# Performance work log

Hardware: AMD Instinct MI355X
Metric: run time of the kernel (lower is better)

The kernel has to match this reference:

```python
import jax, jax.numpy as jnp
import numpy as np


def setup_inputs() -> dict:
    key = jax.random.key(0)
    k1, k2, k3, k4, k5 = jax.random.split(key, 5)
    N, C, H, W = 1, 256, 336, 336
    R, P = 256, 7
    features = jax.random.normal(k1, (N, C, H, W), dtype=jnp.float32)
    # ROIs: integer [x1, y1, x2, y2]; width/height in [P, 63] so every bin is non-empty,
    # and boxes stay inside the feature map.
    x1 = jax.random.randint(k2, (R,), 0, H - 64)
    y1 = jax.random.randint(k3, (R,), 0, H - 64)
    w = jax.random.randint(k4, (R,), P, 64)
    h = jax.random.randint(k5, (R,), P, 64)
    rois = jnp.stack([x1, y1, x1 + w, y1 + h], axis=1).astype(jnp.int32)
    return {"features": features, "rois": rois, "output_size": P}


def _bin_index(lo, size, P, L):
    """For each roi, map every coordinate in [0, L) to its bin index in [0, P), or P if outside.

    Boundaries replicate: int(x1 + (width / P) * w) with float32 division and
    truncation (coords are non-negative, so trunc == floor).
    lo, size: [R] float32.  Returns [R, L] int32.
    """
    ws = jnp.arange(P + 1, dtype=jnp.float32)
    b = jnp.floor(lo[:, None] + (size / P)[:, None] * ws[None, :]).astype(jnp.int32)  # [R, P+1]
    j = jnp.arange(L, dtype=jnp.int32)
    # bin index = number of interior boundaries b[1..P] that are <= j
    cnt = jnp.sum((j[None, None, :] >= b[:, 1:, None]).astype(jnp.int32), axis=1)  # [R, L]
    return jnp.where(j[None, :] < b[:, :1], P, cnt)


def reference(features, rois, output_size):
    P = output_size
    feat = features[0]  # [C, H, W]  (original code requires N == 1)
    C, H, W = feat.shape
    x1 = rois[:, 0].astype(jnp.float32)
    y1 = rois[:, 1].astype(jnp.float32)
    rw = jnp.maximum(rois[:, 2] - rois[:, 0] + 1, 1).astype(jnp.float32)
    rh = jnp.maximum(rois[:, 3] - rois[:, 1] + 1, 1).astype(jnp.float32)
    col_bin = _bin_index(x1, rw, P, W)  # [R, W]
    row_bin = _bin_index(y1, rh, P, H)  # [R, H]

    def pool_one(cb, rb):
        # reduce columns into width-bins: [W, C, H] -> [P+1, C, H], drop 'outside' segment
        t = jax.ops.segment_max(jnp.moveaxis(feat, 2, 0), cb, num_segments=P + 1)[:P]  # [Pw, C, H]
        # reduce rows into height-bins: [H, Pw, C] -> [P+1, Pw, C]
        t = jax.ops.segment_max(jnp.moveaxis(t, 2, 0), rb, num_segments=P + 1)[:P]  # [Ph, Pw, C]
        return jnp.transpose(t, (2, 0, 1))  # [C, Ph, Pw]

    return jax.vmap(pool_one)(col_bin, row_bin)  # [R, C, P, P]
```

## Files before the change

kernel.cpp:

```cpp
#include <hip/hip_runtime.h>
#include <math.h>


#define POOL_P 7

__device__ __forceinline__ float4 max4(float4 a, float4 b) {
  return make_float4(fmaxf(a.x, b.x), fmaxf(a.y, b.y),
                     fmaxf(a.z, b.z), fmaxf(a.w, b.w));
}

__global__ __launch_bounds__(64, 4) void roipool_kernel(
    const float* __restrict__ feat, const int* __restrict__ rois,
    float* __restrict__ out, int C, int H, int W, int R) {
  const int x  = blockIdx.x & 7;
  const int s  = blockIdx.x >> 3;
  const int pass = s / (2 * R);
  const int t    = s - pass * 2 * R;
  const int r    = t >> 1;
  const int half = t & 1;
  const int cg8  = (pass << 3) | x;

  const int lane = threadIdx.x;
  const int k  = lane >> 4;
  const int li = lane & 15;
  const int c0 = (cg8 << 3) + (half << 2);

  const int4 roi = *reinterpret_cast<const int4*>(rois + 4 * r);
  const int x1 = roi.x, y1 = roi.y;
  const int rw = max(roi.z - x1 + 1, 1);
  const int rh = max(roi.w - y1 + 1, 1);
  const int x2 = x1 + rw - 1;

  const float sx = __fdiv_rn((float)rw, (float)POOL_P);
  const float sy = __fdiv_rn((float)rh, (float)POOL_P);
  const float x1f = (float)x1, y1f = (float)y1;

  const int xa = x1 & ~3;
  const bool tailc = (x2 >= xa + 64);
  const int lslot = min((x2 - xa) >> 2, 15);

  const size_t HW = (size_t)H * W;
  const int W4 = W >> 2;
  const float* fck = feat + (size_t)(c0 + k) * HW;
  const float4* pmb = reinterpret_cast<const float4*>(fck + xa) + li;
  const float* pt  = fck + xa + 64;

  __shared__ float stg[4][POOL_P][80];

  const float NEG = -__builtin_inff();

  if (li <= lslot) {
    int hprev = y1;
#pragma unroll
    for (int ph = 0; ph < POOL_P; ++ph) {
      const int hend = (int)__fadd_rn(y1f, __fmul_rn(sy, (float)(ph + 1)));
      const int cnt = hend - hprev;
      const int e84 = (cnt - 1) * 84;
      const float4* q = pmb + (size_t)hprev * W4;
      hprev = hend;
      float4 m = q[0];
      m = max4(m, q[min(84,  e84)]);
      m = max4(m, q[min(168, e84)]);
      m = max4(m, q[min(252, e84)]);
      if (cnt > 4) {
        float4 a = q[336];
        float4 b = q[min(420, e84)];
        float4 c = q[min(504, e84)];
        float4 d = q[min(588, e84)];
        m = max4(m, max4(max4(a, b), max4(c, d)));
      }
      if (cnt > 8) {
        const float4* qq = q + 672;
        for (int h = 8; h < cnt; ++h) { m = max4(m, qq[0]); qq += 84; }
      }
      *reinterpret_cast<float4*>(&stg[k][ph][li << 2]) = m;
    }
  }

  if (tailc && li == 0) {
    int hprev = y1;
#pragma unroll
    for (int ph = 0; ph < POOL_P; ++ph) {
      const int hend = (int)__fadd_rn(y1f, __fmul_rn(sy, (float)(ph + 1)));
      float4 tm = make_float4(NEG, NEG, NEG, NEG);
      for (int h = hprev; h < hend; ++h)
        tm = max4(tm, *reinterpret_cast<const float4*>(pt + (size_t)h * W));
      hprev = hend;
      *reinterpret_cast<float4*>(&stg[k][ph][64]) = tm;
    }
  }

  const size_t ob = ((size_t)r * C + c0) * (POOL_P * POOL_P);
#pragma unroll
  for (int i = lane; i < 4 * POOL_P * POOL_P; i += 64) {
    const int k2 = i / (POOL_P * POOL_P);
    const int j  = i - k2 * (POOL_P * POOL_P);
    const int ph = j / POOL_P;
    const int pw = j - ph * POOL_P;
    const int w0 = (int)__fadd_rn(x1f, __fmul_rn(sx, (float)pw)) - xa;
    const int w1 = (int)__fadd_rn(x1f, __fmul_rn(sx, (float)(pw + 1))) - xa;
    const int a0 = w0 & ~3;
    const float* sq = &stg[k2][ph][a0];
    float4 t0 = *reinterpret_cast<const float4*>(sq);
    float4 t1 = *reinterpret_cast<const float4*>(sq + 4);
    float4 t2 = *reinterpret_cast<const float4*>(sq + 8);
    float4 t3 = *reinterpret_cast<const float4*>(sq + 12);
    const int lo = w0 - a0, hi = w1 - a0;
    float e[16] = {t0.x, t0.y, t0.z, t0.w, t1.x, t1.y, t1.z, t1.w,
                   t2.x, t2.y, t2.z, t2.w, t3.x, t3.y, t3.z, t3.w};
    float m = NEG;
#pragma unroll
    for (int jj = 0; jj < 16; ++jj) {
      const float v = (jj >= lo && jj < hi) ? e[jj] : NEG;
      m = fmaxf(m, v);
    }
    out[ob + i] = m;
  }
}

extern "C" void kernel_launch(void* const* d_in, const int* in_sizes, int n_in,
                              void* d_out, int out_size, void* d_ws, size_t ws_size,
                              hipStream_t stream) {
  const float* feat = (const float*)d_in[0];
  const int*   rois = (const int*)d_in[1];
  float*       out  = (float*)d_out;

  const int C = 256, H = 336, W = 336;
  const int R = in_sizes[1] / 4;

  const int n_cg8 = C / 8;
  dim3 grid(n_cg8 * R * 2), block(64);
  roipool_kernel<<<grid, block, 0, stream>>>(feat, rois, out, C, H, W, R);
}
```

Baseline: 51.06 us.

## Stream ROI rows through an LDS ring with async global_load_lds prefetch

Replaces per-bin direct float4 global loads with a 16-slot LDS ring filled by global_load_lds, keeping 13 rows in flight and counting them with explicit vmcnt waits. Rows are max-reduced as they arrive, and each height bin's width reduction runs as soon as that bin finishes, so the old final pass over a staging array goes away. The aim is to hide memory latency with deeper, steadier prefetch. It removes the lslot guard, so all 16 column slots load even when the ROI is narrow, adding extra traffic. It also relies on hand-placed waitcnts with no barriers, which is fragile within a single wave.

```diff
diff --git a/kernel.cpp b/kernel.cpp
--- a/kernel.cpp
+++ b/kernel.cpp
@@ -3,6 +3,9 @@
 
 
 #define POOL_P 7
+
+typedef __attribute__((address_space(1))) const void gld_src_t;
+typedef __attribute__((address_space(3))) void gld_dst_t;
 
 __device__ __forceinline__ float4 max4(float4 a, float4 b) {
   return make_float4(fmaxf(a.x, b.x), fmaxf(a.y, b.y),
@@ -37,84 +40,98 @@
 
   const int xa = x1 & ~3;
   const bool tailc = (x2 >= xa + 64);
-  const int lslot = min((x2 - xa) >> 2, 15);
 
   const size_t HW = (size_t)H * W;
-  const int W4 = W >> 2;
   const float* fck = feat + (size_t)(c0 + k) * HW;
-  const float4* pmb = reinterpret_cast<const float4*>(fck + xa) + li;
-  const float* pt  = fck + xa + 64;
+  const float* src0 = fck + (size_t)y1 * W + xa + (li << 2);
+  const float* pt   = fck + xa + 64;
 
-  __shared__ float stg[4][POOL_P][80];
+  __shared__ float ring[16][256];
+  __shared__ float colmax[4][80];
+  __shared__ float res[4 * 49];
+  __shared__ float4 tailstg[POOL_P][4];
 
   const float NEG = -__builtin_inff();
+  const float4 NEG4 = make_float4(NEG, NEG, NEG, NEG);
 
-  if (li <= lslot) {
-    int hprev = y1;
-#pragma unroll
-    for (int ph = 0; ph < POOL_P; ++ph) {
-      const int hend = (int)__fadd_rn(y1f, __fmul_rn(sy, (float)(ph + 1)));
-      const int cnt = hend - hprev;
-      const int e84 = (cnt - 1) * 84;
-      const float4* q = pmb + (size_t)hprev * W4;
-      hprev = hend;
-      float4 m = q[0];
-      m = max4(m, q[min(84,  e84)]);
-      m = max4(m, q[min(168, e84)]);
-      m = max4(m, q[min(252, e84)]);
-      if (cnt > 4) {
-        float4 a = q[336];
-        float4 b = q[min(420, e84)];
-        float4 c = q[min(504, e84)];
-        float4 d = q[min(588, e84)];
-        m = max4(m, max4(max4(a, b), max4(c, d)));
-      }
-      if (cnt > 8) {
-        const float4* qq = q + 672;
-        for (int h = 8; h < cnt; ++h) { m = max4(m, qq[0]); qq += 84; }
-      }
-      *reinterpret_cast<float4*>(&stg[k][ph][li << 2]) = m;
-    }
-  }
+  const int b7 = (int)__fadd_rn(y1f, __fmul_rn(sy, (float)POOL_P));
+  const int T  = b7 - y1;
 
   if (tailc && li == 0) {
     int hprev = y1;
 #pragma unroll
     for (int ph = 0; ph < POOL_P; ++ph) {
       const int hend = (int)__fadd_rn(y1f, __fmul_rn(sy, (float)(ph + 1)));
-      float4 tm = make_float4(NEG, NEG, NEG, NEG);
+      float4 tm = NEG4;
       for (int h = hprev; h < hend; ++h)
         tm = max4(tm, *reinterpret_cast<const float4*>(pt + (size_t)h * W));
       hprev = hend;
-      *reinterpret_cast<float4*>(&stg[k][ph][64]) = tm;
+      tailstg[ph][k] = tm;
+    }
+  }
+  asm volatile("s_waitcnt vmcnt(0)" ::: "memory");
+
+#pragma unroll
+  for (int j = 0; j < 13; ++j) {
+    const int rr = min(j, T - 1);
+    __builtin_amdgcn_global_load_lds((gld_src_t*)(src0 + (size_t)rr * W),
+                                     (gld_dst_t*)&ring[j][0], 16, 0, 0);
+  }
+
+  asm volatile("s_waitcnt vmcnt(12)" ::: "memory");
+  float4 v = *reinterpret_cast<const float4*>(&ring[0][lane << 2]);
+
+  int ph = 0;
+  int eoff = (int)__fadd_rn(y1f, __fmul_rn(sy, 1.0f)) - y1;
+  float4 m = NEG4;
+  const size_t ob = ((size_t)r * C + c0) * (POOL_P * POOL_P);
+
+  for (int i = 0; i < T; ++i) {
+    const int nr = min(i + 13, T - 1);
+    __builtin_amdgcn_global_load_lds((gld_src_t*)(src0 + (size_t)nr * W),
+                                     (gld_dst_t*)&ring[(i + 13) & 15][0],
+                                     16, 0, 0);
+    asm volatile("s_waitcnt vmcnt(12)" ::: "memory");
+    const float4 vn =
+        *reinterpret_cast<const float4*>(&ring[(i + 1) & 15][lane << 2]);
+    m = max4(m, v);
+    v = vn;
+
+    if (i + 1 == eoff) {
+      *reinterpret_cast<float4*>(&colmax[k][li << 2]) = m;
+      if (tailc && li == 0)
+        *reinterpret_cast<float4*>(&colmax[k][64]) = tailstg[ph][k];
+      if (lane < 4 * POOL_P) {
+        const int rk  = lane / POOL_P;
+        const int rpw = lane - rk * POOL_P;
+        const int w0 = (int)__fadd_rn(x1f, __fmul_rn(sx, (float)rpw)) - xa;
+        const int w1 = (int)__fadd_rn(x1f, __fmul_rn(sx, (float)(rpw + 1))) - xa;
+        const int a0 = w0 & ~3;
+        const float* sq = &colmax[rk][a0];
+        float4 t0 = *reinterpret_cast<const float4*>(sq);
+        float4 t1 = *reinterpret_cast<const float4*>(sq + 4);
+        float4 t2 = *reinterpret_cast<const float4*>(sq + 8);
+        float4 t3 = *reinterpret_cast<const float4*>(sq + 12);
+        const int lo = w0 - a0, hi = w1 - a0;
+        float e[16] = {t0.x, t0.y, t0.z, t0.w, t1.x, t1.y, t1.z, t1.w,
+                       t2.x, t2.y, t2.z, t2.w, t3.x, t3.y, t3.z, t3.w};
+        float mm = NEG;
+#pragma unroll
+        for (int jj = 0; jj < 16; ++jj) {
+          const float vv = (jj >= lo && jj < hi) ? e[jj] : NEG;
+          mm = fmaxf(mm, vv);
+        }
+        res[rk * 49 + ph * POOL_P + rpw] = mm;
+      }
+      ++ph;
+      eoff = (int)__fadd_rn(y1f, __fmul_rn(sy, (float)(ph + 1))) - y1;
+      m = NEG4;
     }
   }
 
-  const size_t ob = ((size_t)r * C + c0) * (POOL_P * POOL_P);
 #pragma unroll
-  for (int i = lane; i < 4 * POOL_P * POOL_P; i += 64) {
-    const int k2 = i / (POOL_P * POOL_P);
-    const int j  = i - k2 * (POOL_P * POOL_P);
-    const int ph = j / POOL_P;
-    const int pw = j - ph * POOL_P;
-    const int w0 = (int)__fadd_rn(x1f, __fmul_rn(sx, (float)pw)) - xa;
-    const int w1 = (int)__fadd_rn(x1f, __fmul_rn(sx, (float)(pw + 1))) - xa;
-    const int a0 = w0 & ~3;
-    const float* sq = &stg[k2][ph][a0];
-    float4 t0 = *reinterpret_cast<const float4*>(sq);
-    float4 t1 = *reinterpret_cast<const float4*>(sq + 4);
-    float4 t2 = *reinterpret_cast<const float4*>(sq + 8);
-    float4 t3 = *reinterpret_cast<const float4*>(sq + 12);
-    const int lo = w0 - a0, hi = w1 - a0;
-    float e[16] = {t0.x, t0.y, t0.z, t0.w, t1.x, t1.y, t1.z, t1.w,
-                   t2.x, t2.y, t2.z, t2.w, t3.x, t3.y, t3.z, t3.w};
-    float m = NEG;
-#pragma unroll
-    for (int jj = 0; jj < 16; ++jj) {
-      const float v = (jj >= lo && jj < hi) ? e[jj] : NEG;
-      m = fmaxf(m, v);
-    }
-    out[ob + i] = m;
+  for (int i2 = lane; i2 < 4 * POOL_P * POOL_P; i2 += 64) {
+    out[ob + i2] = res[i2];
   }
 }
 
```

Result: slower. 123.6 us (+142.1%).

## Split row reduction across lanes with wave shuffles in 256-thread blocks

Applied to the files above, without the earlier changes.

Blocks grow from one wavefront to four. The rows of each height bin are now spread across four lane groups, and the partial maxima are combined with xor shuffles, so each thread issues far fewer serial loads. A __syncthreads is added before the final column-bin stage, which now gives one output per thread. The change raises parallelism and latency hiding but adds shuffle and barrier overhead. Rows past index 11 are never loaded, which is enough here only because ROI heights are capped at 64, giving at most 10 rows per bin.

```diff
diff --git a/kernel.cpp b/kernel.cpp
--- a/kernel.cpp
+++ b/kernel.cpp
@@ -9,20 +9,28 @@
                      fmaxf(a.z, b.z), fmaxf(a.w, b.w));
 }
 
-__global__ __launch_bounds__(64, 4) void roipool_kernel(
+__device__ __forceinline__ float4 shflx4(float4 v, int mask) {
+  return make_float4(__shfl_xor(v.x, mask, 64), __shfl_xor(v.y, mask, 64),
+                     __shfl_xor(v.z, mask, 64), __shfl_xor(v.w, mask, 64));
+}
+
+__global__ __launch_bounds__(256, 4) void roipool_kernel(
     const float* __restrict__ feat, const int* __restrict__ rois,
     float* __restrict__ out, int C, int H, int W, int R) {
   const int x  = blockIdx.x & 7;
-  const int s  = blockIdx.x >> 3;
-  const int pass = s / (2 * R);
-  const int t    = s - pass * 2 * R;
+  const int s_ = blockIdx.x >> 3;
+  const int pass = s_ / (2 * R);
+  const int t    = s_ - pass * 2 * R;
   const int r    = t >> 1;
   const int half = t & 1;
   const int cg8  = (pass << 3) | x;
 
-  const int lane = threadIdx.x;
-  const int k  = lane >> 4;
-  const int li = lane & 15;
+  const int tid  = threadIdx.x;
+  const int lane = tid & 63;
+  const int w    = tid >> 6;
+  const int jj   = lane >> 4;
+  const int k    = (lane >> 2) & 3;
+  const int sl   = (w << 2) | (lane & 3);
   const int c0 = (cg8 << 3) + (half << 2);
 
   const int4 roi = *reinterpret_cast<const int4*>(rois + 4 * r);
@@ -42,59 +50,51 @@
   const size_t HW = (size_t)H * W;
   const int W4 = W >> 2;
   const float* fck = feat + (size_t)(c0 + k) * HW;
-  const float4* pmb = reinterpret_cast<const float4*>(fck + xa) + li;
-  const float* pt  = fck + xa + 64;
+  const float4* pmb = reinterpret_cast<const float4*>(fck + xa) + sl;
 
   __shared__ float stg[4][POOL_P][80];
 
   const float NEG = -__builtin_inff();
+  const float4 NEG4 = make_float4(NEG, NEG, NEG, NEG);
 
-  if (li <= lslot) {
+  if (sl <= lslot) {
     int hprev = y1;
 #pragma unroll
     for (int ph = 0; ph < POOL_P; ++ph) {
       const int hend = (int)__fadd_rn(y1f, __fmul_rn(sy, (float)(ph + 1)));
       const int cnt = hend - hprev;
-      const int e84 = (cnt - 1) * 84;
+      const int e = cnt - 1;
       const float4* q = pmb + (size_t)hprev * W4;
       hprev = hend;
-      float4 m = q[0];
-      m = max4(m, q[min(84,  e84)]);
-      m = max4(m, q[min(168, e84)]);
-      m = max4(m, q[min(252, e84)]);
-      if (cnt > 4) {
-        float4 a = q[336];
-        float4 b = q[min(420, e84)];
-        float4 c = q[min(504, e84)];
-        float4 d = q[min(588, e84)];
-        m = max4(m, max4(max4(a, b), max4(c, d)));
-      }
-      if (cnt > 8) {
-        const float4* qq = q + 672;
-        for (int h = 8; h < cnt; ++h) { m = max4(m, qq[0]); qq += 84; }
-      }
-      *reinterpret_cast<float4*>(&stg[k][ph][li << 2]) = m;
+      float4 m = q[(size_t)min(jj, e) * W4];
+      if (cnt > 4) m = max4(m, q[(size_t)min(jj + 4, e) * W4]);
+      if (cnt > 8) m = max4(m, q[(size_t)min(jj + 8, e) * W4]);
+      m = max4(m, shflx4(m, 16));
+      m = max4(m, shflx4(m, 32));
+      if (jj == 0)
+        *reinterpret_cast<float4*>(&stg[k][ph][sl << 2]) = m;
     }
   }
 
-  if (tailc && li == 0) {
+  if (tailc && tid < 4) {
+    const float* ptk = feat + (size_t)(c0 + tid) * HW + xa + 64;
     int hprev = y1;
 #pragma unroll
     for (int ph = 0; ph < POOL_P; ++ph) {
       const int hend = (int)__fadd_rn(y1f, __fmul_rn(sy, (float)(ph + 1)));
-      float4 tm = make_float4(NEG, NEG, NEG, NEG);
+      float4 tm = NEG4;
       for (int h = hprev; h < hend; ++h)
-        tm = max4(tm, *reinterpret_cast<const float4*>(pt + (size_t)h * W));
+        tm = max4(tm, *reinterpret_cast<const float4*>(ptk + (size_t)h * W));
       hprev = hend;
-      *reinterpret_cast<float4*>(&stg[k][ph][64]) = tm;
+      *reinterpret_cast<float4*>(&stg[tid][ph][64]) = tm;
     }
   }
 
-  const size_t ob = ((size_t)r * C + c0) * (POOL_P * POOL_P);
-#pragma unroll
-  for (int i = lane; i < 4 * POOL_P * POOL_P; i += 64) {
-    const int k2 = i / (POOL_P * POOL_P);
-    const int j  = i - k2 * (POOL_P * POOL_P);
+  __syncthreads();
+
+  if (tid < 4 * POOL_P * POOL_P) {
+    const int k2 = tid / (POOL_P * POOL_P);
+    const int j  = tid - k2 * (POOL_P * POOL_P);
     const int ph = j / POOL_P;
     const int pw = j - ph * POOL_P;
     const int w0 = (int)__fadd_rn(x1f, __fmul_rn(sx, (float)pw)) - xa;
@@ -110,11 +110,12 @@
                    t2.x, t2.y, t2.z, t2.w, t3.x, t3.y, t3.z, t3.w};
     float m = NEG;
 #pragma unroll
-    for (int jj = 0; jj < 16; ++jj) {
-      const float v = (jj >= lo && jj < hi) ? e[jj] : NEG;
+    for (int jx = 0; jx < 16; ++jx) {
+      const float v = (jx >= lo && jx < hi) ? e[jx] : NEG;
       m = fmaxf(m, v);
     }
-    out[ob + i] = m;
+    const size_t ob = ((size_t)r * C + c0) * (POOL_P * POOL_P);
+    out[ob + tid] = m;
   }
 }
 
@@ -129,6 +130,6 @@
   const int R = in_sizes[1] / 4;
 
   const int n_cg8 = C / 8;
-  dim3 grid(n_cg8 * R * 2), block(64);
+  dim3 grid(n_cg8 * R * 2), block(256);
   roipool_kernel<<<grid, block, 0, stream>>>(feat, rois, out, C, H, W, R);
 }
```

Result: slower. 58.60 us (+14.8%).
